# Kernel optimization log

Hardware: AMD Instinct MI355X
Metric: run time of the kernel (lower is better)

The kernel has to match this reference:

```python
import jax, jax.numpy as jnp
import numpy as np

N_HEAD = 32


def _apply_rope(x, rope):
    # x: (B, H, T, hs); rope: (block_size, hs//2) angles
    B, H, T, hs = x.shape
    ang = rope[:T]  # (T, hs//2)
    cos = jnp.cos(ang)[None, :, None, :]  # (1, T, 1, hs//2)
    sin = jnp.sin(ang)[None, :, None, :]
    xt = x.transpose(0, 2, 1, 3).reshape(B, T, H, hs // 2, 2)
    x0, x1 = xt[..., 0], xt[..., 1]
    out_r = x0 * cos - x1 * sin
    out_i = x0 * sin + x1 * cos
    out = jnp.stack([out_r, out_i], axis=-1).reshape(B, T, H, hs)
    return out.transpose(0, 2, 1, 3)


def setup_inputs() -> dict:
    key = jax.random.key(0)
    ks = jax.random.split(key, 6)
    B, T, C = 2, 2048, 4096
    aT = 10
    hs = C // N_HEAD
    return {
        "x": jax.random.normal(ks[0], (B, T, C), dtype=jnp.float32),
        "adaption_prompt": jax.random.normal(ks[1], (1, aT, C), dtype=jnp.float32),
        "rope_cache": jax.random.uniform(ks[2], (4096, hs // 2), dtype=jnp.float32) * 2.0 * np.pi,
        "w_attn": jax.random.normal(ks[3], (C, 3 * C), dtype=jnp.float32) * 0.02,
        "w_proj": jax.random.normal(ks[4], (C, C), dtype=jnp.float32) * 0.02,
        "gating_factor": jax.random.normal(ks[5], (1,), dtype=jnp.float32) * 0.1,
    }


def reference(x, adaption_prompt, rope_cache, w_attn, w_proj, gating_factor):
    B, T, C = x.shape
    H = N_HEAD
    hs = C // H

    qkv = x @ w_attn  # (B, T, 3C)
    q, k, v = jnp.split(qkv, 3, axis=2)
    q = q.reshape(B, T, H, hs).transpose(0, 2, 1, 3)  # (B, H, T, hs)
    k = k.reshape(B, T, H, hs).transpose(0, 2, 1, 3)
    v = v.reshape(B, T, H, hs).transpose(0, 2, 1, 3)

    q = _apply_rope(q, rope_cache)
    k = _apply_rope(k, rope_cache)

    # causal SDPA, scale = 1/sqrt(head_size)
    scale = 1.0 / jnp.sqrt(jnp.asarray(hs, dtype=q.dtype))
    scores = jnp.einsum("bhqd,bhkd->bhqk", q, k) * scale
    causal = jnp.tril(jnp.ones((T, T), dtype=bool))
    scores = jnp.where(causal[None, None, :, :], scores, jnp.asarray(-jnp.inf, scores.dtype))
    attn = jax.nn.softmax(scores, axis=-1)
    y = jnp.einsum("bhqk,bhkd->bhqd", attn, v)  # (B, H, T, hs)

    # adapter attention (note: scale uses full n_embd, as in source)
    aT = adaption_prompt.shape[1]
    aqkv = adaption_prompt @ w_attn  # (1, aT, 3C)
    _, ak, av = jnp.split(aqkv, 3, axis=2)
    ak = ak.reshape(1, aT, H, hs).transpose(0, 2, 1, 3)  # (1, H, aT, hs)
    av = av.reshape(1, aT, H, hs).transpose(0, 2, 1, 3)
    ascores = jnp.einsum("bhqd,xhkd->bhqk", q, ak) / jnp.sqrt(jnp.asarray(C, q.dtype))
    ascores = gating_factor[0] * jax.nn.softmax(ascores.astype(jnp.float32), axis=-1).astype(q.dtype)
    y = y + jnp.einsum("bhqk,xhkd->bhqd", ascores, av)

    y = y.transpose(0, 2, 1, 3).reshape(B, T, C)
    return y @ w_proj
```

## Files before the change

### kernel.cpp

```cpp
#include <hip/hip_runtime.h>

typedef unsigned short u16;
typedef unsigned int u32;
typedef __attribute__((ext_vector_type(4))) float f32x4;
typedef __attribute__((ext_vector_type(8))) _Float16 half8;
typedef __attribute__((ext_vector_type(8))) unsigned short u16x8;
typedef __attribute__((ext_vector_type(4))) unsigned short u16x4;

static __device__ __forceinline__ u16 f2h(float f) {
  union { _Float16 h; u16 u; } c;
  c.h = (_Float16)f;
  return c.u;
}
static __device__ __forceinline__ float h2f(u16 u) {
  union { _Float16 h; u16 u; } c;
  c.u = u;
  return (float)c.h;
}
static __device__ __forceinline__ void gload_lds16(const void* g, void* l) {
  __builtin_amdgcn_global_load_lds((const __attribute__((address_space(1))) void*)g,
                                   (__attribute__((address_space(3))) void*)l,
                                   16, 0, 0);
}

__global__ __launch_bounds__(256) void transpose_cvt(const float* __restrict__ src,
                                                     u16* __restrict__ dst,
                                                     int R, int C) {
  __shared__ float tile[32][33];
  const int tx = threadIdx.x, ty = threadIdx.y;
  const int c0 = blockIdx.x << 5, r0 = blockIdx.y << 5;
#pragma unroll
  for (int i = 0; i < 32; i += 8)
    tile[ty + i][tx] = src[(size_t)(r0 + ty + i) * C + c0 + tx];
  __syncthreads();
#pragma unroll
  for (int i = 0; i < 32; i += 8)
    dst[(size_t)(c0 + ty + i) * R + r0 + tx] = f2h(tile[tx][ty + i]);
}

__global__ __launch_bounds__(256) void cvt_f32_f16(const float* __restrict__ in,
                                                   u16* __restrict__ out, int n4) {
  int i = blockIdx.x * 256 + threadIdx.x;
  if (i >= n4) return;
  f32x4 v = *(const f32x4*)(in + (size_t)i * 4);
  u16x4 o;
  o[0] = f2h(v[0]); o[1] = f2h(v[1]); o[2] = f2h(v[2]); o[3] = f2h(v[3]);
  *(u16x4*)(out + (size_t)i * 4) = o;
}

static __device__ __forceinline__ void store_out(float* C, size_t idx, float v) { C[idx] = v; }
static __device__ __forceinline__ void store_out(u16* C, size_t idx, float v) { C[idx] = f2h(v); }

template <typename OutT>
__global__ __launch_bounds__(256) void gemm_bt(const u16* __restrict__ A,
                                               const u16* __restrict__ Bt,
                                               OutT* __restrict__ C,
                                               int M, int N, int K) {
  __shared__ u16 As[128 * 64];
  __shared__ u16 Bs[128 * 64];
  const int t = threadIdx.x;
  const int lane = t & 63, w = t >> 6;
  const int g = lane >> 4, l15 = lane & 15;
  const int wr = w >> 1, wc = w & 1;
  const int bm = blockIdx.y, bn = blockIdx.x;
  const u16* Ab = A + (size_t)bm * 128 * K;
  const u16* Bb = Bt + (size_t)bn * 128 * K;
  f32x4 acc[4][4] = {};

  for (int kt = 0; kt < K; kt += 64) {
    __syncthreads();
#pragma unroll
    for (int i = 0; i < 4; ++i) {
      int c = t + 256 * i;
      int row = c >> 3, slot = c & 7;
      gload_lds16(Ab + (size_t)row * K + kt + ((slot ^ (row & 7)) << 3),
                  (char*)As + c * 16);
    }
#pragma unroll
    for (int i = 0; i < 4; ++i) {
      int c = t + 256 * i;
      int row = c >> 3, slot = c & 7;
      gload_lds16(Bb + (size_t)row * K + kt + ((slot ^ (row & 7)) << 3),
                  (char*)Bs + c * 16);
    }
    __syncthreads();
#pragma unroll
    for (int kk = 0; kk < 2; ++kk) {
      half8 a[4], b[4];
#pragma unroll
      for (int m = 0; m < 4; ++m) {
        int row = wr * 64 + m * 16 + l15;
        int slot = (kk * 4 + g) ^ (row & 7);
        a[m] = *(const half8*)((const char*)As + row * 128 + slot * 16);
      }
#pragma unroll
      for (int n = 0; n < 4; ++n) {
        int row = wc * 64 + n * 16 + l15;
        int slot = (kk * 4 + g) ^ (row & 7);
        b[n] = *(const half8*)((const char*)Bs + row * 128 + slot * 16);
      }
#pragma unroll
      for (int m = 0; m < 4; ++m)
#pragma unroll
        for (int n = 0; n < 4; ++n)
          acc[m][n] = __builtin_amdgcn_mfma_f32_16x16x32_f16(a[m], b[n], acc[m][n], 0, 0, 0);
    }
  }
#pragma unroll
  for (int m = 0; m < 4; ++m) {
    int row0 = bm * 128 + wr * 64 + m * 16 + 4 * g;
#pragma unroll
    for (int n = 0; n < 4; ++n) {
      int col = bn * 128 + wc * 64 + n * 16 + l15;
#pragma unroll
      for (int r = 0; r < 4; ++r)
        store_out(C, (size_t)(row0 + r) * N + col, acc[m][n][r]);
    }
  }
}

__global__ __launch_bounds__(256) void rope_kernel(u16* __restrict__ qkv,
                                                   const float* __restrict__ rope) {
  int idx = blockIdx.x * 256 + threadIdx.x;
  int bt = idx >> 12;
  int pp = idx & 4095;
  int part = pp >> 11;
  int within = pp & 2047;
  int hh = within >> 6;
  int p = within & 63;
  int tpos = bt & 2047;
  size_t off = (size_t)bt * 12288 + part * 4096 + hh * 128 + 2 * p;
  u32* ptr = (u32*)(qkv + off);
  u32 v = *ptr;
  float x0 = h2f((u16)(v & 0xffff));
  float x1 = h2f((u16)(v >> 16));
  float sn, cs;
  __sincosf(rope[tpos * 64 + p], &sn, &cs);
  float y0 = x0 * cs - x1 * sn;
  float y1 = x0 * sn + x1 * cs;
  *ptr = (u32)f2h(y0) | ((u32)f2h(y1) << 16);
}

__global__ __launch_bounds__(256) void v_transpose(const u16* __restrict__ qkv,
                                                   u16* __restrict__ vt) {
  __shared__ u16 tile[64 * 128];
  const int bx = blockIdx.x;
  const int tt = bx & 31, h = (bx >> 5) & 31, b = bx >> 10;
  const u16* src = qkv + (size_t)b * 2048 * 12288 + 8192 + h * 128;
  const int t = threadIdx.x;
#pragma unroll
  for (int i = 0; i < 4; ++i) {
    int c = t + 256 * i;
    int row = c >> 4, slot = c & 15;
    u16x8 v = *(const u16x8*)(src + (size_t)(tt * 64 + row) * 12288 + slot * 8);
    *(u16x8*)(tile + row * 128 + ((slot ^ (row >> 3)) << 3)) = v;
  }
  __syncthreads();
  u16* dst = vt + (size_t)(b * 32 + h) * 128 * 2048 + tt * 64;
#pragma unroll
  for (int i = 0; i < 4; ++i) {
    int c = t + 256 * i;
    int drow = c >> 3, t8 = c & 7;
    u16x8 o;
#pragma unroll
    for (int e = 0; e < 8; ++e) {
      int row = t8 * 8 + e;
      int slot = (drow >> 3) ^ (row >> 3);
      o[e] = tile[row * 128 + (slot << 3) + (drow & 7)];
    }
    *(u16x8*)(dst + (size_t)drow * 2048 + t8 * 8) = o;
  }
}

__global__ __launch_bounds__(256) void adaption_kv_kernel(const float* __restrict__ prompt,
                                                          const float* __restrict__ w_attn,
                                                          u16* __restrict__ akbuf,
                                                          u16* __restrict__ avbuf) {
  __shared__ float pl[10][512];
  __shared__ float red[8][10][32];
  const int t = threadIdx.x;
  const int tc = t & 31, tk = t >> 5;
  const int n = blockIdx.x * 32 + tc;
  float acc[10] = {};
  for (int k0 = 0; k0 < 4096; k0 += 512) {
    __syncthreads();
#pragma unroll
    for (int i = 0; i < 20; ++i) {
      int idx = t + 256 * i;
      int j = idx >> 9, kk = idx & 511;
      pl[j][kk] = prompt[(size_t)j * 4096 + k0 + kk];
    }
    __syncthreads();
    for (int kk = tk; kk < 512; kk += 8) {
      float wv = w_attn[(size_t)(k0 + kk) * 12288 + 4096 + n];
#pragma unroll
      for (int j = 0; j < 10; ++j) acc[j] += pl[j][kk] * wv;
    }
  }
  __syncthreads();
#pragma unroll
  for (int j = 0; j < 10; ++j) red[tk][j][tc] = acc[j];
  __syncthreads();
  if (tk == 0) {
    float s[10];
#pragma unroll
    for (int j = 0; j < 10; ++j) {
      s[j] = 0.f;
#pragma unroll
      for (int q = 0; q < 8; ++q) s[j] += red[q][j][tc];
    }
    u16* dst;
    int hh, d;
    if (n < 4096) { dst = akbuf; hh = n >> 7; d = n & 127; }
    else          { dst = avbuf; hh = (n - 4096) >> 7; d = n & 127; }
#pragma unroll
    for (int j = 0; j < 16; ++j)
      dst[(size_t)(hh * 16 + j) * 128 + d] = (j < 10) ? f2h(s[j]) : (u16)0;
  }
}

__global__ __launch_bounds__(256) void attn_kernel(const u16* __restrict__ qkv,
                                                   const u16* __restrict__ vt,
                                                   const u16* __restrict__ akbuf,
                                                   const u16* __restrict__ avbuf,
                                                   const float* __restrict__ gating,
                                                   u16* __restrict__ y) {
  __shared__ u16 Kl[64 * 128];
  __shared__ u16 Vtl[128 * 64];
  __shared__ u16 Pl[4][16 * 64];

  const int t = threadIdx.x;
  const int lane = t & 63, w = t >> 6;
  const int g = lane >> 4, l15 = lane & 15;
  const int bx = blockIdx.x;
  const int qb = 31 - (bx >> 6);
  const int bh = bx & 63, b = bh >> 5, h = bh & 31;
  const int ldq = 12288;
  const u16* Qg = qkv + (size_t)b * 2048 * ldq + h * 128;
  const u16* Kg = Qg + 4096;
  const u16* VtG = vt + (size_t)(b * 32 + h) * 128 * 2048;
  u16* AKb = &Pl[0][0];

#pragma unroll
  for (int i = 0; i < 4; ++i) {
    int c = t + 256 * i;
    int row = c >> 4, slot = c & 15;
    gload_lds16(Qg + (size_t)(qb * 64 + row) * ldq + ((slot ^ (row & 15)) << 3),
                (char*)Kl + c * 16);
  }
  {
    int row = t >> 4, slot = t & 15;
    gload_lds16(akbuf + (size_t)(h * 16 + row) * 128 + ((slot ^ row) << 3),
                (char*)AKb + t * 16);
  }
  __syncthreads();

  half8 qf[4];
#pragma unroll
  for (int kk = 0; kk < 4; ++kk) {
    int slot = (kk * 4 + g) ^ l15;
    qf[kk] = *(const half8*)((const char*)Kl + (w * 16 + l15) * 256 + (slot << 4));
  }
  f32x4 sa = {};
#pragma unroll
  for (int kk = 0; kk < 4; ++kk) {
    int slot = (kk * 4 + g) ^ l15;
    half8 af = *(const half8*)((const char*)AKb + l15 * 256 + (slot << 4));
    sa = __builtin_amdgcn_mfma_f32_16x16x32_f16(qf[kk], af, sa, 0, 0, 0);
  }
  __syncthreads();

  f32x4 acc[8] = {};
  float mrun[4], lrun[4];
#pragma unroll
  for (int r = 0; r < 4; ++r) { mrun[r] = -1e30f; lrun[r] = 0.f; }

  for (int kvt = 0; kvt <= qb; ++kvt) {
#pragma unroll
    for (int i = 0; i < 4; ++i) {
      int c = t + 256 * i;
      int row = c >> 4, slot = c & 15;
      gload_lds16(Kg + (size_t)(kvt * 64 + row) * ldq + ((slot ^ (row & 15)) << 3),
                  (char*)Kl + c * 16);
    }
#pragma unroll
    for (int i = 0; i < 4; ++i) {
      int c = t + 256 * i;
      int d = c >> 3, s3 = c & 7;
      gload_lds16(VtG + (size_t)d * 2048 + kvt * 64 + ((s3 ^ (d & 7)) << 3),
                  (char*)Vtl + c * 16);
    }
    __syncthreads();

    f32x4 s[4] = {};
#pragma unroll
    for (int nf = 0; nf < 4; ++nf) {
#pragma unroll
      for (int kk = 0; kk < 4; ++kk) {
        int slot = (kk * 4 + g) ^ l15;
        half8 kf = *(const half8*)((const char*)Kl + (nf * 16 + l15) * 256 + (slot << 4));
        s[nf] = __builtin_amdgcn_mfma_f32_16x16x32_f16(qf[kk], kf, s[nf], 0, 0, 0);
      }
    }
    const float sc = 0.08838834764831843f;
    if (kvt == qb) {
#pragma unroll
      for (int nf = 0; nf < 4; ++nf)
#pragma unroll
        for (int r = 0; r < 4; ++r) {
          int kv = nf * 16 + l15;
          int qq = w * 16 + 4 * g + r;
          float v = s[nf][r] * sc;
          s[nf][r] = (kv <= qq) ? v : -1e30f;
        }
    } else {
#pragma unroll
      for (int nf = 0; nf < 4; ++nf)
#pragma unroll
        for (int r = 0; r < 4; ++r) s[nf][r] *= sc;
    }

    float alpha[4];
#pragma unroll
    for (int r = 0; r < 4; ++r) {
      float mt = fmaxf(fmaxf(s[0][r], s[1][r]), fmaxf(s[2][r], s[3][r]));
#pragma unroll
      for (int off = 1; off < 16; off <<= 1)
        mt = fmaxf(mt, __shfl_xor(mt, off, 64));
      float mn = fmaxf(mrun[r], mt);
      alpha[r] = __expf(mrun[r] - mn);
      mrun[r] = mn;
      float rs = 0.f;
#pragma unroll
      for (int nf = 0; nf < 4; ++nf) {
        float p = __expf(s[nf][r] - mn);
        s[nf][r] = p;
        rs += p;
      }
#pragma unroll
      for (int off = 1; off < 16; off <<= 1)
        rs += __shfl_xor(rs, off, 64);
      lrun[r] = lrun[r] * alpha[r] + rs;
    }
#pragma unroll
    for (int nd = 0; nd < 8; ++nd)
#pragma unroll
      for (int r = 0; r < 4; ++r)
        acc[nd][r] *= alpha[r];

#pragma unroll
    for (int nf = 0; nf < 4; ++nf)
#pragma unroll
      for (int r = 0; r < 4; ++r) {
        int qq = 4 * g + r;
        int kv = nf * 16 + l15;
        int byteoff = (qq * 128 + kv * 2) ^ ((qq & 7) << 4);
        *(u16*)((char*)Pl[w] + byteoff) = f2h(s[nf][r]);
      }

#pragma unroll
    for (int kk2 = 0; kk2 < 2; ++kk2) {
      int pslot = (kk2 * 4 + g) ^ (l15 & 7);
      half8 pf = *(const half8*)((const char*)Pl[w] + l15 * 128 + (pslot << 4));
#pragma unroll
      for (int nd = 0; nd < 8; ++nd) {
        int d = nd * 16 + l15;
        int slot = (kk2 * 4 + g) ^ (d & 7);
        half8 vf = *(const half8*)((const char*)Vtl + d * 128 + (slot << 4));
        acc[nd] = __builtin_amdgcn_mfma_f32_16x16x32_f16(pf, vf, acc[nd], 0, 0, 0);
      }
    }
    __syncthreads();
  }

  {
    int d = t >> 1;
    int jb = (t & 1) << 4;
#pragma unroll
    for (int i = 0; i < 16; ++i) {
      int j = jb + i;
      u16 v = (j < 16) ? avbuf[(size_t)(h * 16 + j) * 128 + d] : (u16)0;
      int byteoff = (d * 64 + j * 2) ^ ((d & 3) << 4);
      *(u16*)((char*)Kl + byteoff) = v;
    }
  }
  __syncthreads();

  float ga = gating[0];
  float pa4[4];
#pragma unroll
  for (int r = 0; r < 4; ++r) {
    float v = sa[r] * (1.0f / 64.0f);
    if (l15 >= 10) v = -1e30f;
    float mt = v;
#pragma unroll
    for (int off = 1; off < 16; off <<= 1)
      mt = fmaxf(mt, __shfl_xor(mt, off, 64));
    float p = __expf(v - mt);
    float rs = p;
#pragma unroll
    for (int off = 1; off < 16; off <<= 1)
      rs += __shfl_xor(rs, off, 64);
    pa4[r] = p / rs * ga;
  }
#pragma unroll
  for (int r = 0; r < 4; ++r) {
    float inv = 1.0f / lrun[r];
#pragma unroll
    for (int nd = 0; nd < 8; ++nd)
      acc[nd][r] *= inv;
  }
#pragma unroll
  for (int r = 0; r < 4; ++r) {
    int qq = 4 * g + r;
    int b1 = (qq * 128 + l15 * 2) ^ ((qq & 7) << 4);
    *(u16*)((char*)Pl[w] + b1) = f2h(pa4[r]);
    int b2 = (qq * 128 + (16 + l15) * 2) ^ ((qq & 7) << 4);
    *(u16*)((char*)Pl[w] + b2) = 0;
  }
  {
    int pslot = g ^ (l15 & 7);
    half8 pf = *(const half8*)((const char*)Pl[w] + l15 * 128 + (pslot << 4));
#pragma unroll
    for (int nd = 0; nd < 8; ++nd) {
      int d = nd * 16 + l15;
      int byteoff = (d * 64 + g * 16) ^ ((d & 3) << 4);
      half8 avf = *(const half8*)((const char*)Kl + byteoff);
      acc[nd] = __builtin_amdgcn_mfma_f32_16x16x32_f16(pf, avf, acc[nd], 0, 0, 0);
    }
  }
#pragma unroll
  for (int nd = 0; nd < 8; ++nd) {
    int col = h * 128 + nd * 16 + l15;
#pragma unroll
    for (int r = 0; r < 4; ++r) {
      int row = qb * 64 + w * 16 + 4 * g + r;
      y[(size_t)(b * 2048 + row) * 4096 + col] = f2h(acc[nd][r]);
    }
  }
}

extern "C" void kernel_launch(void* const* d_in, const int* in_sizes, int n_in,
                              void* d_out, int out_size, void* d_ws, size_t ws_size,
                              hipStream_t stream) {
  (void)in_sizes; (void)n_in; (void)out_size; (void)ws_size;
  const float* x      = (const float*)d_in[0];
  const float* prompt = (const float*)d_in[1];
  const float* rope   = (const float*)d_in[2];
  const float* w_attn = (const float*)d_in[3];
  const float* w_proj = (const float*)d_in[4];
  const float* gating = (const float*)d_in[5];
  float* out = (float*)d_out;

  char* ws = (char*)d_ws;
  u16* WtA = (u16*)(ws);
  u16* Yb  = (u16*)(ws);
  u16* VtG = (u16*)(ws + 33554432);
  u16* qkv = (u16*)(ws + 100663296);
  u16* xb  = (u16*)(ws + 201326592);
  u16* WtP = (u16*)(ws + 201326592);
  u16* akb = (u16*)(ws + 234881024);
  u16* avb = (u16*)(ws + 234881024 + 131072);

  transpose_cvt<<<dim3(384, 128), dim3(32, 8), 0, stream>>>(w_attn, WtA, 4096, 12288);
  cvt_f32_f16<<<dim3(16384), dim3(256), 0, stream>>>(x, xb, 4194304);
  gemm_bt<u16><<<dim3(96, 32), dim3(256), 0, stream>>>(xb, WtA, qkv, 4096, 12288, 4096);
  rope_kernel<<<dim3(65536), dim3(256), 0, stream>>>(qkv, rope);
  v_transpose<<<dim3(2048), dim3(256), 0, stream>>>(qkv, VtG);
  adaption_kv_kernel<<<dim3(256), dim3(256), 0, stream>>>(prompt, w_attn, akb, avb);
  attn_kernel<<<dim3(2048), dim3(256), 0, stream>>>(qkv, VtG, akb, avb, gating, Yb);
  transpose_cvt<<<dim3(128, 128), dim3(32, 8), 0, stream>>>(w_proj, WtP, 4096, 4096);
  gemm_bt<float><<<dim3(32, 32), dim3(256), 0, stream>>>(Yb, WtP, out, 4096, 4096, 4096);
}
```

Measured before the change: 1.132 ms.

## Replace 128x128 GEMM with 256x256 eight-wave pipelined GEMM using double-buffered LDS

Swaps the simple single-buffered 128x128 tile GEMM for a 256x256 tile kernel with 8 waves. It double-buffers K-slices in LDS and splits each slice into four phases that interleave global-to-LDS prefetch with MFMA work, using s_setprio and explicit vmcnt waits. It also remaps block IDs to group workgroups for L2 locality. The aim is to hide global load latency, raise arithmetic intensity per tile and remove the full __syncthreads stalls. In exchange it uses 128KB of LDS and many more accumulator registers, and its hand-written wait counts must match the order of the issued loads.

```diff
diff --git a/kernel.cpp b/kernel.cpp
--- a/kernel.cpp
+++ b/kernel.cpp
@@ -51,70 +51,110 @@
 static __device__ __forceinline__ void store_out(float* C, size_t idx, float v) { C[idx] = v; }
 static __device__ __forceinline__ void store_out(u16* C, size_t idx, float v) { C[idx] = f2h(v); }
 
+static __device__ __forceinline__ void stageA(const u16* __restrict__ Ab, int K, int kt,
+                                              u16* As, int mh, int t) {
+#pragma unroll
+  for (int i = 0; i < 2; ++i) {
+    int row = i * 128 + mh * 64 + (t >> 3);
+    int slot = t & 7;
+    gload_lds16(Ab + (size_t)row * K + kt + ((slot ^ (row & 7)) << 3),
+                (char*)As + (size_t)(i * 128 + mh * 64) * 128 + t * 16);
+  }
+}
+static __device__ __forceinline__ void stageB(const u16* __restrict__ Bb, int K, int kt,
+                                              u16* Bs, int nh, int t) {
+#pragma unroll
+  for (int i = 0; i < 2; ++i) {
+    int j = (t >> 8) + 2 * i;
+    int rem = t & 255;
+    int row = j * 64 + nh * 32 + (rem >> 3);
+    int slot = rem & 7;
+    gload_lds16(Bb + (size_t)row * K + kt + ((slot ^ (row & 7)) << 3),
+                (char*)Bs + (size_t)(j * 64 + nh * 32) * 128 + rem * 16);
+  }
+}
+
+#define DO_PHASE(AS, BS, MH, NH, STAGE_STMT, WAIT_STR)                           \
+  {                                                                              \
+    half8 af[4][2], bf[2][2];                                                    \
+    _Pragma("unroll") for (int mf = 0; mf < 4; ++mf)                             \
+      _Pragma("unroll") for (int kk = 0; kk < 2; ++kk) {                         \
+        int row = wm * 128 + ((MH) * 4 + mf) * 16 + l15;                         \
+        int slot = (kk * 4 + g) ^ (l15 & 7);                                     \
+        af[mf][kk] = *(const half8*)((const char*)(AS) + row * 128 + slot * 16); \
+      }                                                                          \
+    _Pragma("unroll") for (int nf = 0; nf < 2; ++nf)                             \
+      _Pragma("unroll") for (int kk = 0; kk < 2; ++kk) {                         \
+        int row = wn * 64 + ((NH) * 2 + nf) * 16 + l15;                          \
+        int slot = (kk * 4 + g) ^ (l15 & 7);                                     \
+        bf[nf][kk] = *(const half8*)((const char*)(BS) + row * 128 + slot * 16); \
+      }                                                                          \
+    STAGE_STMT;                                                                  \
+    asm volatile("s_barrier" ::: "memory");                                      \
+    __builtin_amdgcn_s_setprio(1);                                               \
+    _Pragma("unroll") for (int kk = 0; kk < 2; ++kk)                             \
+      _Pragma("unroll") for (int mf = 0; mf < 4; ++mf)                           \
+        _Pragma("unroll") for (int nf = 0; nf < 2; ++nf)                         \
+          acc[(MH) * 4 + mf][(NH) * 2 + nf] =                                    \
+              __builtin_amdgcn_mfma_f32_16x16x32_f16(                            \
+                  af[mf][kk], bf[nf][kk], acc[(MH) * 4 + mf][(NH) * 2 + nf],     \
+                  0, 0, 0);                                                      \
+    __builtin_amdgcn_s_setprio(0);                                               \
+    asm volatile(WAIT_STR ::: "memory");                                         \
+  }
+
 template <typename OutT>
-__global__ __launch_bounds__(256) void gemm_bt(const u16* __restrict__ A,
-                                               const u16* __restrict__ Bt,
-                                               OutT* __restrict__ C,
-                                               int M, int N, int K) {
-  __shared__ u16 As[128 * 64];
-  __shared__ u16 Bs[128 * 64];
+__global__ __launch_bounds__(512, 2) void gemm256(const u16* __restrict__ A,
+                                                  const u16* __restrict__ Bt,
+                                                  OutT* __restrict__ C,
+                                                  int M, int N, int K, int nbn) {
+  __shared__ u16 lds[4][16384];
   const int t = threadIdx.x;
-  const int lane = t & 63, w = t >> 6;
+  const int lane = t & 63;
+  const int wid = t >> 6;
   const int g = lane >> 4, l15 = lane & 15;
-  const int wr = w >> 1, wc = w & 1;
-  const int bm = blockIdx.y, bn = blockIdx.x;
-  const u16* Ab = A + (size_t)bm * 128 * K;
-  const u16* Bb = Bt + (size_t)bn * 128 * K;
-  f32x4 acc[4][4] = {};
-
-  for (int kt = 0; kt < K; kt += 64) {
-    __syncthreads();
-#pragma unroll
-    for (int i = 0; i < 4; ++i) {
-      int c = t + 256 * i;
-      int row = c >> 3, slot = c & 7;
-      gload_lds16(Ab + (size_t)row * K + kt + ((slot ^ (row & 7)) << 3),
-                  (char*)As + c * 16);
-    }
-#pragma unroll
-    for (int i = 0; i < 4; ++i) {
-      int c = t + 256 * i;
-      int row = c >> 3, slot = c & 7;
-      gload_lds16(Bb + (size_t)row * K + kt + ((slot ^ (row & 7)) << 3),
-                  (char*)Bs + c * 16);
-    }
-    __syncthreads();
-#pragma unroll
-    for (int kk = 0; kk < 2; ++kk) {
-      half8 a[4], b[4];
-#pragma unroll
-      for (int m = 0; m < 4; ++m) {
-        int row = wr * 64 + m * 16 + l15;
-        int slot = (kk * 4 + g) ^ (row & 7);
-        a[m] = *(const half8*)((const char*)As + row * 128 + slot * 16);
-      }
-#pragma unroll
-      for (int n = 0; n < 4; ++n) {
-        int row = wc * 64 + n * 16 + l15;
-        int slot = (kk * 4 + g) ^ (row & 7);
-        b[n] = *(const half8*)((const char*)Bs + row * 128 + slot * 16);
-      }
-#pragma unroll
-      for (int m = 0; m < 4; ++m)
-#pragma unroll
-        for (int n = 0; n < 4; ++n)
-          acc[m][n] = __builtin_amdgcn_mfma_f32_16x16x32_f16(a[m], b[n], acc[m][n], 0, 0, 0);
-    }
-  }
-#pragma unroll
-  for (int m = 0; m < 4; ++m) {
-    int row0 = bm * 128 + wr * 64 + m * 16 + 4 * g;
-#pragma unroll
-    for (int n = 0; n < 4; ++n) {
-      int col = bn * 128 + wc * 64 + n * 16 + l15;
+  const int wm = wid >> 2, wn = wid & 3;
+  const int nwg = gridDim.x;
+  const int bid = blockIdx.x;
+  const int wgid = (bid & 7) * (nwg >> 3) + (bid >> 3);
+  const int bm = wgid / nbn, bn = wgid % nbn;
+  const u16* Ab = A + (size_t)bm * 256 * K;
+  const u16* Bb = Bt + (size_t)bn * 256 * K;
+  f32x4 acc[8][4] = {};
+
+  stageB(Bb, K, 0, lds[1], 0, t);
+  stageA(Ab, K, 0, lds[0], 0, t);
+  stageB(Bb, K, 0, lds[1], 1, t);
+  stageA(Ab, K, 0, lds[0], 1, t);
+  stageB(Bb, K, 64, lds[3], 0, t);
+  stageA(Ab, K, 64, lds[2], 0, t);
+  asm volatile("s_waitcnt vmcnt(4)\ns_barrier" ::: "memory");
+
+  const int nit = K >> 7;
+  for (int i = 0; i < nit; ++i) {
+    int k1 = (2 * i + 1) << 6;
+    int k2 = (2 * i + 2) << 6; if (k2 >= K) k2 = 0;
+    int k3 = (2 * i + 3) << 6; if (k3 >= K) k3 = 0;
+    DO_PHASE(lds[0], lds[1], 0, 0, stageB(Bb, K, k1, lds[3], 1, t), "s_waitcnt vmcnt(6)\ns_barrier");
+    DO_PHASE(lds[0], lds[1], 1, 0, stageA(Ab, K, k1, lds[2], 1, t), "s_barrier");
+    DO_PHASE(lds[0], lds[1], 0, 1, stageB(Bb, K, k2, lds[1], 0, t), "s_barrier");
+    DO_PHASE(lds[0], lds[1], 1, 1, stageA(Ab, K, k2, lds[0], 0, t), "s_waitcnt vmcnt(8)\ns_barrier");
+    DO_PHASE(lds[2], lds[3], 0, 0, stageB(Bb, K, k2, lds[1], 1, t), "s_waitcnt vmcnt(6)\ns_barrier");
+    DO_PHASE(lds[2], lds[3], 1, 0, stageA(Ab, K, k2, lds[0], 1, t), "s_barrier");
+    DO_PHASE(lds[2], lds[3], 0, 1, stageB(Bb, K, k3, lds[3], 0, t), "s_barrier");
+    DO_PHASE(lds[2], lds[3], 1, 1, stageA(Ab, K, k3, lds[2], 0, t), "s_waitcnt vmcnt(8)\ns_barrier");
+  }
+  asm volatile("s_waitcnt vmcnt(0)" ::: "memory");
+
+#pragma unroll
+  for (int mf = 0; mf < 8; ++mf) {
+    int row0 = bm * 256 + wm * 128 + mf * 16 + 4 * g;
+#pragma unroll
+    for (int nf = 0; nf < 4; ++nf) {
+      int col = bn * 256 + wn * 64 + nf * 16 + l15;
 #pragma unroll
       for (int r = 0; r < 4; ++r)
-        store_out(C, (size_t)(row0 + r) * N + col, acc[m][n][r]);
+        store_out(C, (size_t)(row0 + r) * N + col, acc[mf][nf][r]);
     }
   }
 }
@@ -464,11 +504,11 @@
 
   transpose_cvt<<<dim3(384, 128), dim3(32, 8), 0, stream>>>(w_attn, WtA, 4096, 12288);
   cvt_f32_f16<<<dim3(16384), dim3(256), 0, stream>>>(x, xb, 4194304);
-  gemm_bt<u16><<<dim3(96, 32), dim3(256), 0, stream>>>(xb, WtA, qkv, 4096, 12288, 4096);
+  gemm256<u16><<<dim3(768), dim3(512), 0, stream>>>(xb, WtA, qkv, 4096, 12288, 4096, 48);
   rope_kernel<<<dim3(65536), dim3(256), 0, stream>>>(qkv, rope);
   v_transpose<<<dim3(2048), dim3(256), 0, stream>>>(qkv, VtG);
   adaption_kv_kernel<<<dim3(256), dim3(256), 0, stream>>>(prompt, w_attn, akb, avb);
   attn_kernel<<<dim3(2048), dim3(256), 0, stream>>>(qkv, VtG, akb, avb, gating, Yb);
   transpose_cvt<<<dim3(128, 128), dim3(32, 8), 0, stream>>>(w_proj, WtP, 4096, 4096);
-  gemm_bt<float><<<dim3(32, 32), dim3(256), 0, stream>>>(Yb, WtP, out, 4096, 4096, 4096);
-}
+  gemm256<float><<<dim3(256), dim3(512), 0, stream>>>(Yb, WtP, out, 4096, 4096, 4096, 16);
+}
```

New measurement: 1.049 ms. -7.3%, faster.
